# Kernel optimization log

Hardware: AMD Instinct MI355X
Metric: run time of the kernel (lower is better)

The kernel has to match this reference:

```python
import jax, jax.numpy as jnp
import numpy as np

B, S, D, H = 2, 2048, 1024, 16
DK = D // H


def setup_inputs() -> dict:
    key = jax.random.key(0)
    ks = jax.random.split(key, 7)
    return {
        "query": jax.random.normal(ks[0], (B, S, D), jnp.float32),
        "key": jax.random.normal(ks[1], (B, S, D), jnp.float32),
        "value": jax.random.normal(ks[2], (B, S, D), jnp.float32),
        "w_q": jax.random.normal(ks[3], (D, D), jnp.float32) * (1.0 / np.sqrt(D)),
        "w_k": jax.random.normal(ks[4], (D, D), jnp.float32) * (1.0 / np.sqrt(D)),
        "w_v": jax.random.normal(ks[5], (D, D), jnp.float32) * (1.0 / np.sqrt(D)),
        "w_o": jax.random.normal(ks[6], (D, D), jnp.float32) * (1.0 / np.sqrt(D)),
    }


def reference(query, key, value, w_q, w_k, w_v, w_o):
    # Linear(bias=False) in torch computes x @ W.T where W is [out, in].
    Q = jnp.einsum('bsd,ed->bse', query, w_q)
    K = jnp.einsum('bsd,ed->bse', key, w_k)
    V = jnp.einsum('bsd,ed->bse', value, w_v)
    # split heads: [B, H, S, DK]
    Q = Q.reshape(B, S, H, DK).transpose(0, 2, 1, 3)
    K = K.reshape(B, S, H, DK).transpose(0, 2, 1, 3)
    V = V.reshape(B, S, H, DK).transpose(0, 2, 1, 3)
    scale = 1.0 / np.sqrt(DK).astype(np.float32)
    scores = jnp.einsum('bhqd,bhkd->bhqk', Q, K) * scale  # [B,H,S,S]
    attn = jax.nn.softmax(scores, axis=-1)
    context = jnp.einsum('bhqk,bhkd->bhqd', attn, V)
    context = context.transpose(0, 2, 1, 3).reshape(B, S, D)
    return jnp.einsum('bsd,ed->bse', context, w_o)
```

## Files before the change

### kernel.cpp

```cpp
#include <hip/hip_runtime.h>

typedef unsigned short u16;
typedef unsigned int u32;
typedef __bf16 bf16x8 __attribute__((ext_vector_type(8)));
typedef float f32x4 __attribute__((ext_vector_type(4)));
typedef short s16x4 __attribute__((ext_vector_type(4)));

#define AS1 __attribute__((address_space(1)))
#define AS3 __attribute__((address_space(3)))

__device__ __forceinline__ f32x4 mfma16(bf16x8 a, bf16x8 b, f32x4 c) {
    return __builtin_amdgcn_mfma_f32_16x16x32_bf16(a, b, c, 0, 0, 0);
}
__device__ __forceinline__ f32x4 mfma16k16(s16x4 a, s16x4 b, f32x4 c) {
    return __builtin_amdgcn_mfma_f32_16x16x16bf16_1k(a, b, c, 0, 0, 0);
}

__device__ __forceinline__ u16 f2bf(float f) {
    return __builtin_bit_cast(u16, (__bf16)f);
}

__device__ __forceinline__ void gld16(const u16* g, u16* l) {
    __builtin_amdgcn_global_load_lds((AS1 void*)g, (AS3 void*)l, 16, 0, 0);
}

__device__ __forceinline__ void barrier_nodrain() {
    asm volatile("s_waitcnt lgkmcnt(0)" ::: "memory");
    __builtin_amdgcn_s_barrier();
    asm volatile("" ::: "memory");
}

__global__ __launch_bounds__(256) void cvt_all(const float* __restrict__ q, const float* __restrict__ k,
                                               const float* __restrict__ v, const float* __restrict__ wq,
                                               const float* __restrict__ wk, const float* __restrict__ wv,
                                               const float* __restrict__ wo, u16* __restrict__ qo,
                                               u16* __restrict__ ko, u16* __restrict__ vo,
                                               u16* __restrict__ wqo, u16* __restrict__ wko,
                                               u16* __restrict__ wvo, u16* __restrict__ woo) {
    const int y = blockIdx.y;
    const float* x; u16* o; int n;
    switch (y) {
        case 0: x = q; o = qo; n = 4 << 20; break;
        case 1: x = k; o = ko; n = 4 << 20; break;
        case 2: x = v; o = vo; n = 4 << 20; break;
        case 3: x = wq; o = wqo; n = 1 << 20; break;
        case 4: x = wk; o = wko; n = 1 << 20; break;
        case 5: x = wv; o = wvo; n = 1 << 20; break;
        default: x = wo; o = woo; n = 1 << 20; break;
    }
    int i = (blockIdx.x * 256 + threadIdx.x) * 4;
    if (i >= n) return;
    float4 vv = *(const float4*)(x + i);
    u32 lo = (u32)f2bf(vv.x) | ((u32)f2bf(vv.y) << 16);
    u32 hi = (u32)f2bf(vv.z) | ((u32)f2bf(vv.w) << 16);
    *(uint2*)(o + i) = make_uint2(lo, hi);
}

template <int BM, int BN, bool BF16OUT>
__device__ __forceinline__ void gemm_core(const u16* __restrict__ A, const u16* __restrict__ Bt,
                                          void* __restrict__ Cp, int K, int N, int m0, int n0,
                                          float oscale) {
    constexpr int WROWS = BM / 64;
    constexpr int WCOLS = 4 / WROWS;
    constexpr int BFR = BN / WCOLS / 16;
    constexpr int RPWA = BM / 4;
    constexpr int RPWB = BN / 4;
    constexpr int PA = RPWA / 8, PB = RPWB / 8;
    __shared__ __align__(16) u16 As[BM * 64];
    __shared__ __align__(16) u16 Bs[BN * 64];
    const int tid = threadIdx.x;
    const int lane = tid & 63, wave = tid >> 6;
    const int l16 = lane & 15, q4 = lane >> 4;
    const int wm = (wave / WCOLS) * 64, wn = (wave % WCOLS) * (BFR * 16);

    const f32x4 fz = {0.f, 0.f, 0.f, 0.f};
    f32x4 acc[4][BFR];
#pragma unroll
    for (int i = 0; i < 4; ++i)
#pragma unroll
        for (int j = 0; j < BFR; ++j) acc[i][j] = fz;

    const int srow = lane >> 3;
    const int clog = (lane & 7) ^ srow;
    const u16* Ag = A + (size_t)(m0 + wave * RPWA + srow) * K + clog * 8;
    const u16* Bg = Bt + (size_t)(n0 + wave * RPWB + srow) * K + clog * 8;
    const int rk = l16 & 7;

    for (int k0 = 0; k0 < K; k0 += 64) {
        __syncthreads();
#pragma unroll
        for (int p = 0; p < PA; ++p)
            gld16(Ag + (size_t)(p * 8) * K + k0, As + (wave * RPWA + p * 8) * 64);
#pragma unroll
        for (int p = 0; p < PB; ++p)
            gld16(Bg + (size_t)(p * 8) * K + k0, Bs + (wave * RPWB + p * 8) * 64);
        __syncthreads();
#pragma unroll
        for (int h = 0; h < 2; ++h) {
            const int cs = ((h * 4 + q4) ^ rk) * 8;
            bf16x8 af[4], bfr[BFR];
#pragma unroll
            for (int i = 0; i < 4; ++i)
                af[i] = *(const bf16x8*)&As[(wm + i * 16 + l16) * 64 + cs];
#pragma unroll
            for (int j = 0; j < BFR; ++j)
                bfr[j] = *(const bf16x8*)&Bs[(wn + j * 16 + l16) * 64 + cs];
#pragma unroll
            for (int i = 0; i < 4; ++i)
#pragma unroll
                for (int j = 0; j < BFR; ++j) acc[i][j] = mfma16(af[i], bfr[j], acc[i][j]);
        }
    }

#pragma unroll
    for (int i = 0; i < 4; ++i) {
        const int row = m0 + wm + i * 16 + q4 * 4;
#pragma unroll
        for (int j = 0; j < BFR; ++j) {
            const int col = n0 + wn + j * 16 + l16;
#pragma unroll
            for (int r = 0; r < 4; ++r) {
                const float vr = acc[i][j][r] * oscale;
                if constexpr (BF16OUT)
                    ((u16*)Cp)[(size_t)(row + r) * N + col] = f2bf(vr);
                else
                    ((float*)Cp)[(size_t)(row + r) * N + col] = vr;
            }
        }
    }
}

__global__ __launch_bounds__(256) void gemm_qkv(const u16* __restrict__ qb, const u16* __restrict__ kb,
                                                const u16* __restrict__ vb, const u16* __restrict__ wqb,
                                                const u16* __restrict__ wkb, const u16* __restrict__ wvb,
                                                u16* __restrict__ Qp, u16* __restrict__ Kp,
                                                u16* __restrict__ VtAll) {
    const int z = blockIdx.y;
    int x = blockIdx.x;
    if (z != 2) x = (x & 7) * 32 + (x >> 3);
    const u16 *A, *Bt;
    u16* C;
    int N, m0, n0;
    float sc = 1.0f;
    if (z == 0) {
        A = qb; Bt = wqb; C = Qp; N = 1024; m0 = (x >> 3) * 128; n0 = (x & 7) * 128;
        sc = 0.18033688011112042f;
    } else if (z == 1) {
        A = kb; Bt = wkb; C = Kp; N = 1024; m0 = (x >> 3) * 128; n0 = (x & 7) * 128;
    } else {
        A = wvb; Bt = vb; C = VtAll; N = 4096; m0 = (x >> 5) * 128; n0 = (x & 31) * 128;
    }
    gemm_core<128, 128, true>(A, Bt, C, 1024, N, m0, n0, sc);
}

__global__ __launch_bounds__(256) void gemm_out(const u16* __restrict__ ctx,
                                                const u16* __restrict__ wob,
                                                float* __restrict__ out) {
    const int xo = (blockIdx.x & 7) * 64 + (blockIdx.x >> 3);
    gemm_core<64, 128, false>(ctx, wob, out, 1024, 1024, (xo >> 3) * 64, (xo & 7) * 128, 1.0f);
}

__global__ __launch_bounds__(512, 4) void flash_attn(const u16* __restrict__ Qp,
                                                     const u16* __restrict__ Kp,
                                                     const u16* __restrict__ VtAll,
                                                     u16* __restrict__ Ctx) {
    constexpr int D = 1024, SS = 2048, LD = 72;
    __shared__ __align__(16) u16 Ks[2][64 * LD];
    __shared__ __align__(16) u16 Vts[2][64 * LD];

    const int tid = threadIdx.x;
    const int lane = tid & 63, wave = tid >> 6;
    const int l16 = lane & 15, q4 = lane >> 4;

    const int nb = blockIdx.x;
    const int orig = (nb & 7) * 64 + (nb >> 3);
    const int h = (orig >> 4) & 15, b = orig >> 8;
    const int q0 = (orig & 15) * 128 + wave * 16;

    bf16x8 qf[2];
    {
        const u16* Qb = Qp + (size_t)(b * SS + q0 + l16) * D + h * 64;
        qf[0] = *(const bf16x8*)(Qb + q4 * 8);
        qf[1] = *(const bf16x8*)(Qb + 32 + q4 * 8);
    }

    const f32x4 fz = {0.f, 0.f, 0.f, 0.f};
    f32x4 ot[4], lacc = fz;
#pragma unroll
    for (int dt = 0; dt < 4; ++dt) ot[dt] = fz;

    s16x4 onesA;
    onesA[0] = onesA[1] = onesA[2] = onesA[3] = (short)0x3F80;

    const int sr = tid >> 3;
    const int scol = (tid & 7) * 8;
    const int vswap = (sr >> 3) & 1;
    const int swV = (l16 >> 3) & 1;
    const u16* Kg = Kp + (size_t)(b * SS + sr) * D + h * 64 + scol;
    const u16* Vg = VtAll + (size_t)(h * 64 + sr) * 4096 + b * SS + scol;

    uint4 kv, vv;
    auto prefetch = [&](int kt) {
        kv = *(const uint4*)(Kg + (size_t)kt * D);
        vv = *(const uint4*)(Vg + kt);
    };
    auto stage = [&](int buf) {
        uint4 w = vswap ? make_uint4(vv.z, vv.w, vv.x, vv.y) : vv;
        *(uint4*)&Ks[buf][sr * LD + scol] = kv;
        *(uint4*)&Vts[buf][sr * LD + scol] = w;
    };

    prefetch(0);
    for (int kt = 0; kt < SS; kt += 64) {
        const int buf = (kt >> 6) & 1;
        stage(buf);
        const int nk = (kt + 64 < SS) ? kt + 64 : 0;
        prefetch(nk);
        barrier_nodrain();

        f32x4 st[4];
        __builtin_amdgcn_s_setprio(1);
#pragma unroll
        for (int nt = 0; nt < 4; ++nt) {
            const bf16x8 ka = *(const bf16x8*)&Ks[buf][(nt * 16 + l16) * LD + q4 * 8];
            const bf16x8 kb2 = *(const bf16x8*)&Ks[buf][(nt * 16 + l16) * LD + 32 + q4 * 8];
            f32x4 s = mfma16(ka, qf[0], fz);
            st[nt] = mfma16(kb2, qf[1], s);
        }
        __builtin_amdgcn_s_setprio(0);

        s16x4 p[4];
#pragma unroll
        for (int nt = 0; nt < 4; ++nt) {
#pragma unroll
            for (int r = 0; r < 4; ++r)
                p[nt][r] = (short)f2bf(__builtin_amdgcn_exp2f(st[nt][r]));
        }

        __builtin_amdgcn_s_setprio(1);
#pragma unroll
        for (int nt = 0; nt < 4; ++nt) {
#pragma unroll
            for (int dt = 0; dt < 4; ++dt) {
                const s16x4 va =
                    *(const s16x4*)&Vts[buf][(dt * 16 + l16) * LD + ((nt * 4 + q4) ^ swV) * 4];
                ot[dt] = mfma16k16(va, p[nt], ot[dt]);
            }
            lacc = mfma16k16(onesA, p[nt], lacc);
        }
        __builtin_amdgcn_s_setprio(0);
    }

    {
        const float inv = 1.f / lacc[0];
        u16* Cb = Ctx + (size_t)(b * SS + q0 + l16) * D + h * 64 + q4 * 4;
#pragma unroll
        for (int dt = 0; dt < 4; ++dt) {
            s16x4 w;
#pragma unroll
            for (int r = 0; r < 4; ++r) w[r] = (short)f2bf(ot[dt][r] * inv);
            *(s16x4*)(Cb + dt * 16) = w;
        }
    }
}

extern "C" void kernel_launch(void* const* d_in, const int* in_sizes, int n_in,
                              void* d_out, int out_size, void* d_ws, size_t ws_size,
                              hipStream_t stream) {
    const float* query = (const float*)d_in[0];
    const float* key   = (const float*)d_in[1];
    const float* value = (const float*)d_in[2];
    const float* w_q   = (const float*)d_in[3];
    const float* w_k   = (const float*)d_in[4];
    const float* w_v   = (const float*)d_in[5];
    const float* w_o   = (const float*)d_in[6];
    float* out = (float*)d_out;

    const size_t MEG = 1024 * 1024;
    if (ws_size < 64 * MEG) return;
    u16* ws = (u16*)d_ws;
    u16* qb    = ws;
    u16* kb    = ws + 4 * MEG;
    u16* vb    = ws + 8 * MEG;
    u16* wqb   = ws + 12 * MEG;
    u16* wkb   = ws + 13 * MEG;
    u16* wvb   = ws + 14 * MEG;
    u16* wob   = ws + 15 * MEG;
    u16* Qp    = ws + 16 * MEG;
    u16* Kp    = ws + 20 * MEG;
    u16* VtAll = ws + 24 * MEG;
    u16* ctx   = ws + 28 * MEG;

    cvt_all<<<dim3(4096, 7), 256, 0, stream>>>(query, key, value, w_q, w_k, w_v, w_o,
                                               qb, kb, vb, wqb, wkb, wvb, wob);
    gemm_qkv<<<dim3(256, 3), 256, 0, stream>>>(qb, kb, vb, wqb, wkb, wvb, Qp, Kp, VtAll);
    flash_attn<<<dim3(512), 512, 0, stream>>>(Qp, Kp, VtAll, ctx);
    gemm_out<<<dim3(512), 256, 0, stream>>>(ctx, wob, out);
}
```

Baseline: 212.0 us.

## Fuse fp32-to-bf16 activation conversion into QKV projection GEMM loads

Removes the separate conversion pass over the q/k/v activations. The QKV GEMM now reads fp32 activations directly, packs them to bf16 in registers, and stores them into double-buffered padded LDS with register prefetch, replacing the global_load_lds path. This avoids writing and re-reading 24MB of bf16 intermediates. In exchange it loads twice the bytes per A/B tile inside the GEMM, uses more registers, and repeats the conversion for each tile that reads the same rows.

```diff
diff --git a/kernel.cpp b/kernel.cpp
--- a/kernel.cpp
+++ b/kernel.cpp
@@ -24,36 +24,127 @@
     __builtin_amdgcn_global_load_lds((AS1 void*)g, (AS3 void*)l, 16, 0, 0);
 }
 
+__device__ __forceinline__ uint4 pack8(float4 a, float4 b) {
+    return make_uint4((u32)f2bf(a.x) | ((u32)f2bf(a.y) << 16),
+                      (u32)f2bf(a.z) | ((u32)f2bf(a.w) << 16),
+                      (u32)f2bf(b.x) | ((u32)f2bf(b.y) << 16),
+                      (u32)f2bf(b.z) | ((u32)f2bf(b.w) << 16));
+}
+
 __device__ __forceinline__ void barrier_nodrain() {
     asm volatile("s_waitcnt lgkmcnt(0)" ::: "memory");
     __builtin_amdgcn_s_barrier();
     asm volatile("" ::: "memory");
 }
 
-__global__ __launch_bounds__(256) void cvt_all(const float* __restrict__ q, const float* __restrict__ k,
-                                               const float* __restrict__ v, const float* __restrict__ wq,
-                                               const float* __restrict__ wk, const float* __restrict__ wv,
-                                               const float* __restrict__ wo, u16* __restrict__ qo,
-                                               u16* __restrict__ ko, u16* __restrict__ vo,
-                                               u16* __restrict__ wqo, u16* __restrict__ wko,
-                                               u16* __restrict__ wvo, u16* __restrict__ woo) {
+__global__ __launch_bounds__(256) void cvt_w(const float* __restrict__ wq, const float* __restrict__ wk,
+                                             const float* __restrict__ wv, const float* __restrict__ wo,
+                                             u16* __restrict__ wqo, u16* __restrict__ wko,
+                                             u16* __restrict__ wvo, u16* __restrict__ woo) {
     const int y = blockIdx.y;
-    const float* x; u16* o; int n;
+    const float* x; u16* o;
     switch (y) {
-        case 0: x = q; o = qo; n = 4 << 20; break;
-        case 1: x = k; o = ko; n = 4 << 20; break;
-        case 2: x = v; o = vo; n = 4 << 20; break;
-        case 3: x = wq; o = wqo; n = 1 << 20; break;
-        case 4: x = wk; o = wko; n = 1 << 20; break;
-        case 5: x = wv; o = wvo; n = 1 << 20; break;
-        default: x = wo; o = woo; n = 1 << 20; break;
-    }
-    int i = (blockIdx.x * 256 + threadIdx.x) * 4;
-    if (i >= n) return;
+        case 0: x = wq; o = wqo; break;
+        case 1: x = wk; o = wko; break;
+        case 2: x = wv; o = wvo; break;
+        default: x = wo; o = woo; break;
+    }
+    const int i = (blockIdx.x * 256 + threadIdx.x) * 4;
     float4 vv = *(const float4*)(x + i);
     u32 lo = (u32)f2bf(vv.x) | ((u32)f2bf(vv.y) << 16);
     u32 hi = (u32)f2bf(vv.z) | ((u32)f2bf(vv.w) << 16);
     *(uint2*)(o + i) = make_uint2(lo, hi);
+}
+
+template <bool AF32, bool BF32>
+__device__ __forceinline__ void gemm_rs(const void* __restrict__ Apv, const void* __restrict__ Btv,
+                                        u16* __restrict__ Cp, int K, int N, int m0, int n0,
+                                        float oscale) {
+    constexpr int LDT = 72;
+    __shared__ __align__(16) u16 As[2][128 * LDT];
+    __shared__ __align__(16) u16 Bs[2][128 * LDT];
+    const int tid = threadIdx.x;
+    const int lane = tid & 63, wave = tid >> 6;
+    const int l16 = lane & 15, q4 = lane >> 4;
+    const int wm = (wave >> 1) * 64, wn = (wave & 1) * 64;
+
+    const f32x4 fz = {0.f, 0.f, 0.f, 0.f};
+    f32x4 acc[4][4];
+#pragma unroll
+    for (int i = 0; i < 4; ++i)
+#pragma unroll
+        for (int j = 0; j < 4; ++j) acc[i][j] = fz;
+
+    const int sr = tid >> 3, pos = (tid & 7) * 8;
+    const float* Af = (const float*)Apv + (size_t)(m0 + sr) * K + pos;
+    const u16*   Ab = (const u16*)Apv + (size_t)(m0 + sr) * K + pos;
+    const float* Bf = (const float*)Btv + (size_t)(n0 + sr) * K + pos;
+    const u16*   Bb = (const u16*)Btv + (size_t)(n0 + sr) * K + pos;
+
+    float4 pa[4][2], pb[4][2];
+    uint4 qa[4], qb[4];
+    auto prefetch = [&](int k0) {
+#pragma unroll
+        for (int p = 0; p < 4; ++p) {
+            const size_t ro = (size_t)(p * 32) * K + k0;
+            if constexpr (AF32) {
+                pa[p][0] = *(const float4*)(Af + ro);
+                pa[p][1] = *(const float4*)(Af + ro + 4);
+            } else {
+                qa[p] = *(const uint4*)(Ab + ro);
+            }
+            if constexpr (BF32) {
+                pb[p][0] = *(const float4*)(Bf + ro);
+                pb[p][1] = *(const float4*)(Bf + ro + 4);
+            } else {
+                qb[p] = *(const uint4*)(Bb + ro);
+            }
+        }
+    };
+    auto stage = [&](int buf) {
+#pragma unroll
+        for (int p = 0; p < 4; ++p) {
+            uint4 wa, wb;
+            if constexpr (AF32) wa = pack8(pa[p][0], pa[p][1]); else wa = qa[p];
+            if constexpr (BF32) wb = pack8(pb[p][0], pb[p][1]); else wb = qb[p];
+            *(uint4*)&As[buf][(sr + p * 32) * LDT + pos] = wa;
+            *(uint4*)&Bs[buf][(sr + p * 32) * LDT + pos] = wb;
+        }
+    };
+
+    prefetch(0);
+    for (int k0 = 0; k0 < K; k0 += 64) {
+        const int buf = (k0 >> 6) & 1;
+        stage(buf);
+        prefetch(k0 + 64 < K ? k0 + 64 : 0);
+        barrier_nodrain();
+#pragma unroll
+        for (int h = 0; h < 2; ++h) {
+            bf16x8 af[4], bfr[4];
+#pragma unroll
+            for (int i = 0; i < 4; ++i)
+                af[i] = *(const bf16x8*)&As[buf][(wm + i * 16 + l16) * LDT + (h * 4 + q4) * 8];
+#pragma unroll
+            for (int j = 0; j < 4; ++j)
+                bfr[j] = *(const bf16x8*)&Bs[buf][(wn + j * 16 + l16) * LDT + (h * 4 + q4) * 8];
+#pragma unroll
+            for (int i = 0; i < 4; ++i)
+#pragma unroll
+                for (int j = 0; j < 4; ++j) acc[i][j] = mfma16(af[i], bfr[j], acc[i][j]);
+        }
+    }
+
+#pragma unroll
+    for (int i = 0; i < 4; ++i) {
+        const int row = m0 + wm + i * 16 + q4 * 4;
+#pragma unroll
+        for (int j = 0; j < 4; ++j) {
+            const int col = n0 + wn + j * 16 + l16;
+#pragma unroll
+            for (int r = 0; r < 4; ++r)
+                Cp[(size_t)(row + r) * N + col] = f2bf(acc[i][j][r] * oscale);
+        }
+    }
 }
 
 template <int BM, int BN, bool BF16OUT>
@@ -130,27 +221,22 @@
     }
 }
 
-__global__ __launch_bounds__(256) void gemm_qkv(const u16* __restrict__ qb, const u16* __restrict__ kb,
-                                                const u16* __restrict__ vb, const u16* __restrict__ wqb,
+__global__ __launch_bounds__(256) void gemm_qkv(const float* __restrict__ q, const float* __restrict__ k,
+                                                const float* __restrict__ v, const u16* __restrict__ wqb,
                                                 const u16* __restrict__ wkb, const u16* __restrict__ wvb,
                                                 u16* __restrict__ Qp, u16* __restrict__ Kp,
                                                 u16* __restrict__ VtAll) {
     const int z = blockIdx.y;
     int x = blockIdx.x;
     if (z != 2) x = (x & 7) * 32 + (x >> 3);
-    const u16 *A, *Bt;
-    u16* C;
-    int N, m0, n0;
-    float sc = 1.0f;
     if (z == 0) {
-        A = qb; Bt = wqb; C = Qp; N = 1024; m0 = (x >> 3) * 128; n0 = (x & 7) * 128;
-        sc = 0.18033688011112042f;
+        gemm_rs<true, false>(q, wqb, Qp, 1024, 1024, (x >> 3) * 128, (x & 7) * 128,
+                             0.18033688011112042f);
     } else if (z == 1) {
-        A = kb; Bt = wkb; C = Kp; N = 1024; m0 = (x >> 3) * 128; n0 = (x & 7) * 128;
+        gemm_rs<true, false>(k, wkb, Kp, 1024, 1024, (x >> 3) * 128, (x & 7) * 128, 1.0f);
     } else {
-        A = wvb; Bt = vb; C = VtAll; N = 4096; m0 = (x >> 5) * 128; n0 = (x & 31) * 128;
-    }
-    gemm_core<128, 128, true>(A, Bt, C, 1024, N, m0, n0, sc);
+        gemm_rs<false, true>(wvb, v, VtAll, 1024, 4096, (x >> 5) * 128, (x & 31) * 128, 1.0f);
+    }
 }
 
 __global__ __launch_bounds__(256) void gemm_out(const u16* __restrict__ ctx,
@@ -277,23 +363,19 @@
     float* out = (float*)d_out;
 
     const size_t MEG = 1024 * 1024;
-    if (ws_size < 64 * MEG) return;
+    if (ws_size < 40 * MEG) return;
     u16* ws = (u16*)d_ws;
-    u16* qb    = ws;
-    u16* kb    = ws + 4 * MEG;
-    u16* vb    = ws + 8 * MEG;
-    u16* wqb   = ws + 12 * MEG;
-    u16* wkb   = ws + 13 * MEG;
-    u16* wvb   = ws + 14 * MEG;
-    u16* wob   = ws + 15 * MEG;
-    u16* Qp    = ws + 16 * MEG;
-    u16* Kp    = ws + 20 * MEG;
-    u16* VtAll = ws + 24 * MEG;
-    u16* ctx   = ws + 28 * MEG;
-
-    cvt_all<<<dim3(4096, 7), 256, 0, stream>>>(query, key, value, w_q, w_k, w_v, w_o,
-                                               qb, kb, vb, wqb, wkb, wvb, wob);
-    gemm_qkv<<<dim3(256, 3), 256, 0, stream>>>(qb, kb, vb, wqb, wkb, wvb, Qp, Kp, VtAll);
+    u16* wqb   = ws;
+    u16* wkb   = ws + 1 * MEG;
+    u16* wvb   = ws + 2 * MEG;
+    u16* wob   = ws + 3 * MEG;
+    u16* Qp    = ws + 4 * MEG;
+    u16* Kp    = ws + 8 * MEG;
+    u16* VtAll = ws + 12 * MEG;
+    u16* ctx   = ws + 16 * MEG;
+
+    cvt_w<<<dim3(1024, 4), 256, 0, stream>>>(w_q, w_k, w_v, w_o, wqb, wkb, wvb, wob);
+    gemm_qkv<<<dim3(256, 3), 256, 0, stream>>>(query, key, value, wqb, wkb, wvb, Qp, Kp, VtAll);
     flash_attn<<<dim3(512), 512, 0, stream>>>(Qp, Kp, VtAll, ctx);
     gemm_out<<<dim3(512), 256, 0, stream>>>(ctx, wob, out);
 }
```

After: 221.4 us. 4.4% more time.
